# Kernel optimization log

Hardware: AMD Instinct MI355X
Metric: run time of the kernel (lower is better)

## Reference

```python
import jax, jax.numpy as jnp
import numpy as np

H, D = 8, 16
NA, NB, E, F = 50000, 50000, 200000, 128
SQRT_D = float(np.sqrt(D))


def _proj(x, W, b):
    # Linear then split heads: [N, F] -> [N, H, D]
    return (x @ W + b).reshape(x.shape[0], H, D)


def _seg_softmax(alpha, idx, n):
    # softmax over edges sharing the same destination node (per head)
    amax = jax.ops.segment_max(alpha, idx, num_segments=n)
    amax = jnp.where(jnp.isfinite(amax), amax, 0.0)
    ex = jnp.exp(alpha - amax[idx])
    den = jax.ops.segment_sum(ex, idx, num_segments=n)
    return ex / (den[idx] + 1e-16)


def _hgt_conv(xa, xb, eis, Wk, bk, Wq, bq, Wv, bv, Wa, ba, skip, arel, mrel, prel):
    # node types: 0='a', 1='b'; edge types: 0 a->b, 1 b->a, 2 a->a
    xs = (xa, xb)
    k = [_proj(xs[t], Wk[t], bk[t]) for t in range(2)]
    q = [_proj(xs[t], Wq[t], bq[t]) for t in range(2)]
    v = [_proj(xs[t], Wv[t], bv[t]) for t in range(2)]
    nn_ = (xa.shape[0], xb.shape[0])
    agg = [jnp.zeros((nn_[t], H, D), xa.dtype) for t in range(2)]
    spec = ((0, 1, eis[0]), (1, 0, eis[1]), (0, 0, eis[2]))
    for e, (s, d, ei) in enumerate(spec):
        src, dst = ei[0], ei[1]
        k_rel = jnp.einsum('nhd,hde->nhe', k[s], arel[e])  # [Ns,H,D]
        v_rel = jnp.einsum('nhd,hde->nhe', v[s], mrel[e])
        alpha = jnp.sum(q[d][dst] * k_rel[src], axis=-1) * prel[e] / SQRT_D  # [E,H]
        w = _seg_softmax(alpha, dst, nn_[d])
        agg[d] = agg[d] + jax.ops.segment_sum(v_rel[src] * w[..., None], dst, num_segments=nn_[d])
    outs = []
    for t in range(2):
        o = jax.nn.gelu(agg[t].reshape(-1, H * D), approximate=False) @ Wa[t] + ba[t]
        sgate = jax.nn.sigmoid(skip[t])  # learned skip-gate, dims match so always applied
        outs.append(sgate * o + (1.0 - sgate) * xs[t])
    return outs[0], outs[1]


def _forward(xa, xb, eis, Wk, bk, Wq, bq, Wv, bv, Wa, ba, skip, arel, mrel, prel):
    for l in range(2):
        xa, xb = _hgt_conv(xa, xb, eis, Wk[l], bk[l], Wq[l], bq[l], Wv[l], bv[l],
                           Wa[l], ba[l], skip[l], arel[l], mrel[l], prel[l])
        if l < 1:
            xa, xb = jax.nn.relu(xa), jax.nn.relu(xb)  # dropout: identity in eval mode
    return xa, xb


def setup_inputs() -> dict:
    key = jax.random.key(0)
    ks = jax.random.split(key, 12)
    s = 0.05
    return {
        'xa': jax.random.normal(ks[0], (NA, F), jnp.float32),
        'xb': jax.random.normal(ks[1], (NB, F), jnp.float32),
        'ei_ab': jax.random.randint(ks[2], (2, E), 0, NA, dtype=jnp.int32),
        'ei_ba': jax.random.randint(ks[3], (2, E), 0, NB, dtype=jnp.int32),
        'ei_aa': jax.random.randint(ks[4], (2, E), 0, NA, dtype=jnp.int32),
        'Wk': jax.random.normal(ks[5], (2, 2, F, F), jnp.float32) * s,
        'bk': jnp.zeros((2, 2, F), jnp.float32),
        'Wq': jax.random.normal(ks[6], (2, 2, F, F), jnp.float32) * s,
        'bq': jnp.zeros((2, 2, F), jnp.float32),
        'Wv': jax.random.normal(ks[7], (2, 2, F, F), jnp.float32) * s,
        'bv': jnp.zeros((2, 2, F), jnp.float32),
        'Wa': jax.random.normal(ks[8], (2, 2, F, F), jnp.float32) * s,
        'ba': jnp.zeros((2, 2, F), jnp.float32),
        'skip': jnp.zeros((2, 2), jnp.float32),
        'arel': jax.random.normal(ks[9], (2, 3, H, D, D), jnp.float32) * (1.0 / SQRT_D),
        'mrel': jax.random.normal(ks[10], (2, 3, H, D, D), jnp.float32) * (1.0 / SQRT_D),
        'prel': jnp.ones((2, 3, H), jnp.float32),
    }


def reference(xa, xb, ei_ab, ei_ba, ei_aa, Wk, bk, Wq, bq, Wv, bv, Wa, ba, skip, arel, mrel, prel):
    return _forward(xa, xb, (ei_ab, ei_ba, ei_aa), Wk, bk, Wq, bq, Wv, bv, Wa, ba, skip, arel, mrel, prel)
```

## Files before the change

kernel.cpp:

```cpp
#include <hip/hip_runtime.h>
#include <hip/hip_bf16.h>
#include <math.h>

#define F 128
#define NH 8
#define HD 16

static inline int cdiv(int a, int b) { return (a + b - 1) / b; }

typedef __attribute__((ext_vector_type(8))) short bf16x8;
typedef __attribute__((ext_vector_type(4))) float f32x4;

__device__ __forceinline__ float geluf(float x) {
    return 0.5f * x * (1.f + erff(x * 0.70710678118654752440f));
}

__device__ __forceinline__ short f2bf(float f) {
    __hip_bfloat16 h = __float2bfloat16(f);
    return *reinterpret_cast<short*>(&h);
}

__device__ __forceinline__ float bflo(unsigned int u) { return __uint_as_float(u << 16); }
__device__ __forceinline__ float bfhi(unsigned int u) { return __uint_as_float(u & 0xffff0000u); }
__device__ __forceinline__ float bf2f(short s) {
    return __uint_as_float(((unsigned int)(unsigned short)s) << 16);
}

__device__ __forceinline__ void slot_info(int slot, int& kind, int& wsel, int& e, int& t) {
    switch (slot) {
        case 0: kind = 0; wsel = 0; t = 0; e = 0; break;
        case 1: kind = 1; wsel = 1; t = 0; e = 0; break;
        case 2: kind = 1; wsel = 2; t = 0; e = 0; break;
        case 3: kind = 1; wsel = 1; t = 0; e = 2; break;
        case 4: kind = 1; wsel = 2; t = 0; e = 2; break;
        case 5: kind = 0; wsel = 0; t = 1; e = 0; break;
        case 6: kind = 1; wsel = 1; t = 1; e = 1; break;
        case 7: kind = 1; wsel = 2; t = 1; e = 1; break;
        case 8: kind = 0; wsel = 3; t = 0; e = 0; break;
        default: kind = 0; wsel = 3; t = 1; e = 0; break;
    }
}

__global__ void prep_weights(const float* __restrict__ Wk, const float* __restrict__ bk,
                             const float* __restrict__ Wq, const float* __restrict__ bq,
                             const float* __restrict__ Wv, const float* __restrict__ bv,
                             const float* __restrict__ Wa, const float* __restrict__ ba,
                             const float* __restrict__ arel, const float* __restrict__ mrel,
                             short* __restrict__ Wslots, float* __restrict__ bslots) {
    const int WTOT = 10 * 16384;
    const int layer = blockIdx.y;
    short* Wl = Wslots + (size_t)layer * WTOT;
    float* bl = bslots + (size_t)layer * 10 * 128;
    int idx = blockIdx.x * blockDim.x + threadIdx.x;
    if (idx < WTOT) {
        int slot = idx >> 14, rem = idx & 16383;
        int n = rem >> 7, k = rem & 127;
        int kind, wsel, e, t;
        slot_info(slot, kind, wsel, e, t);
        float out;
        if (kind == 0) {
            const float* Wb = (wsel == 0 ? Wq : Wa) + (size_t)(layer * 2 + t) * 16384;
            out = Wb[k * 128 + n];
        } else {
            int h = n >> 4, j = n & 15;
            const float* Wb = (wsel == 1 ? Wk : Wv) + (size_t)(layer * 2 + t) * 16384;
            const float* R = (wsel == 1 ? arel : mrel) + (size_t)((layer * 3 + e) * NH + h) * 256;
            float s = 0.f;
            #pragma unroll
            for (int d = 0; d < HD; ++d) s += Wb[k * 128 + h * 16 + d] * R[d * 16 + j];
            out = s;
        }
        Wl[(size_t)slot * 16384 + n * 128 + k] = f2bf(out);
    } else {
        int r = idx - WTOT;
        if (r < 10 * 128) {
            int slot = r >> 7, n = r & 127;
            int kind, wsel, e, t;
            slot_info(slot, kind, wsel, e, t);
            float out;
            if (kind == 0) {
                const float* bb = (wsel == 0 ? bq : ba) + (size_t)(layer * 2 + t) * 128;
                out = bb[n];
            } else {
                int h = n >> 4, j = n & 15;
                const float* bb = (wsel == 1 ? bk : bv) + (size_t)(layer * 2 + t) * 128;
                const float* R = (wsel == 1 ? arel : mrel) + (size_t)((layer * 3 + e) * NH + h) * 256;
                float s = 0.f;
                #pragma unroll
                for (int d = 0; d < HD; ++d) s += bb[h * 16 + d] * R[d * 16 + j];
                out = s;
            }
            bl[slot * 128 + n] = out;
        }
    }
}

template <typename AT>
__global__ __launch_bounds__(256) void gemm_qkv_all(
    const AT* __restrict__ Aa, const AT* __restrict__ Ab,
    const short* __restrict__ Wl, const float* __restrict__ bl,
    short* __restrict__ qA, short* __restrict__ kvA0, short* __restrict__ kvA2,
    short* __restrict__ qB, short* __restrict__ kvB1,
    int NA_, int NB_, int nbA) {
    __shared__ short Ws[128 * 136];
    __shared__ short As[64 * 136];
    float* Wsf = (float*)Ws;
    const int tid = threadIdx.x;
    const int bid = blockIdx.x;
    const int side = bid >= nbA;
    const AT* A = side ? Ab : Aa;
    const int N = side ? NB_ : NA_;
    const int row0 = (side ? bid - nbA : bid) * 64;
    const short* Wbase = Wl + (side ? (size_t)5 * 16384 : 0);
    const float* bbase = bl + (side ? 5 * 128 : 0);
    const int S = side ? 3 : 5;

    #pragma unroll
    for (int it = 0; it < 4; ++it) {
        int chunk = tid + it * 256;
        int r = chunk >> 4, c8 = (chunk & 15) * 8;
        int gr = row0 + r;
        bf16x8 s = {};
        if (gr < N) {
            if constexpr (sizeof(AT) == 4) {
                float4 v0 = *(const float4*)&A[(size_t)gr * F + c8];
                float4 v1 = *(const float4*)&A[(size_t)gr * F + c8 + 4];
                s[0] = f2bf(v0.x); s[1] = f2bf(v0.y); s[2] = f2bf(v0.z); s[3] = f2bf(v0.w);
                s[4] = f2bf(v1.x); s[5] = f2bf(v1.y); s[6] = f2bf(v1.z); s[7] = f2bf(v1.w);
            } else {
                s = *(const bf16x8*)&A[(size_t)gr * F + c8];
            }
        }
        *(bf16x8*)&As[r * 136 + c8] = s;
    }
    __syncthreads();

    const int wave = tid >> 6;
    const int lane = tid & 63;
    const int m16 = lane & 15;
    const int kg = lane >> 4;
    const int arow = wave * 16 + m16;

    bf16x8 af[4];
    #pragma unroll
    for (int kq = 0; kq < 4; ++kq)
        af[kq] = *(const bf16x8*)&As[arow * 136 + kq * 32 + kg * 8];

    for (int s = 0; s < S; ++s) {
        if (s) __syncthreads();
        const short* Wt = Wbase + (size_t)s * 16384;
        #pragma unroll
        for (int it = 0; it < 8; ++it) {
            int chunk = tid + it * 256;
            int r = chunk >> 4, c8 = (chunk & 15) * 8;
            *(int4*)&Ws[r * 136 + c8] = *(const int4*)&Wt[r * 128 + c8];
        }
        __syncthreads();

        f32x4 acc[8] = {};
        #pragma unroll
        for (int kq = 0; kq < 4; ++kq) {
            #pragma unroll
            for (int nt = 0; nt < 8; ++nt) {
                bf16x8 b = *(const bf16x8*)&Ws[(nt * 16 + m16) * 136 + kq * 32 + kg * 8];
                acc[nt] = __builtin_amdgcn_mfma_f32_16x16x32_bf16(af[kq], b, acc[nt], 0, 0, 0);
            }
        }
        __syncthreads();

        #pragma unroll
        for (int nt = 0; nt < 8; ++nt)
            #pragma unroll
            for (int r = 0; r < 4; ++r)
                Wsf[(wave * 16 + kg * 4 + r) * 132 + nt * 16 + m16] = acc[nt][r];
        __syncthreads();

        short* optr; int old, ooff;
        if (side) {
            if (s == 0)      { optr = qB;   old = 128; ooff = 0; }
            else if (s == 1) { optr = kvB1; old = 256; ooff = 0; }
            else             { optr = kvB1; old = 256; ooff = 128; }
        } else {
            if (s == 0)      { optr = qA;   old = 128; ooff = 0; }
            else if (s == 1) { optr = kvA0; old = 256; ooff = 0; }
            else if (s == 2) { optr = kvA0; old = 256; ooff = 128; }
            else if (s == 3) { optr = kvA2; old = 256; ooff = 0; }
            else             { optr = kvA2; old = 256; ooff = 128; }
        }
        const float* bias = bbase + s * 128;
        #pragma unroll
        for (int it = 0; it < 4; ++it) {
            int chunk = tid + it * 256;
            int r = chunk >> 4, c8 = (chunk & 15) * 8;
            int gr = row0 + r;
            if (gr >= N) continue;
            float4 b0 = *(const float4*)&bias[c8];
            float4 b1 = *(const float4*)&bias[c8 + 4];
            bf16x8 o;
            o[0] = f2bf(Wsf[r * 132 + c8 + 0] + b0.x);
            o[1] = f2bf(Wsf[r * 132 + c8 + 1] + b0.y);
            o[2] = f2bf(Wsf[r * 132 + c8 + 2] + b0.z);
            o[3] = f2bf(Wsf[r * 132 + c8 + 3] + b0.w);
            o[4] = f2bf(Wsf[r * 132 + c8 + 4] + b1.x);
            o[5] = f2bf(Wsf[r * 132 + c8 + 5] + b1.y);
            o[6] = f2bf(Wsf[r * 132 + c8 + 6] + b1.z);
            o[7] = f2bf(Wsf[r * 132 + c8 + 7] + b1.w);
            *(bf16x8*)&optr[(size_t)gr * old + ooff + c8] = o;
        }
    }
}

template <int OMODE>
__global__ __launch_bounds__(256) void gemm_out_all(
    const short* __restrict__ aggA, const short* __restrict__ aggB,
    const short* __restrict__ Wl, const float* __restrict__ bl,
    const float* __restrict__ xfA, const float* __restrict__ xfB,
    const short* __restrict__ xbA, const short* __restrict__ xbB,
    const float* __restrict__ skipp,
    float* __restrict__ CfA, float* __restrict__ CfB,
    short* __restrict__ CbA, short* __restrict__ CbB,
    int NA_, int NB_, int nbA) {
    __shared__ short Ws[128 * 136];
    __shared__ short As[64 * 136];
    float* Wsf = (float*)Ws;
    const int tid = threadIdx.x;
    const int bid = blockIdx.x;
    const int side = bid >= nbA;
    const short* A = side ? aggB : aggA;
    const int N = side ? NB_ : NA_;
    const int row0 = (side ? bid - nbA : bid) * 64;
    const short* Wt = Wl + (size_t)(side ? 9 : 8) * 16384;
    const float* bias = bl + (side ? 9 : 8) * 128;

    #pragma unroll
    for (int it = 0; it < 8; ++it) {
        int chunk = tid + it * 256;
        int r = chunk >> 4, c8 = (chunk & 15) * 8;
        *(int4*)&Ws[r * 136 + c8] = *(const int4*)&Wt[r * 128 + c8];
    }
    #pragma unroll
    for (int it = 0; it < 4; ++it) {
        int chunk = tid + it * 256;
        int r = chunk >> 4, c8 = (chunk & 15) * 8;
        int gr = row0 + r;
        bf16x8 s = {};
        if (gr < N) {
            s = *(const bf16x8*)&A[(size_t)gr * F + c8];
            #pragma unroll
            for (int u = 0; u < 8; ++u) s[u] = f2bf(geluf(bf2f(s[u])));
        }
        *(bf16x8*)&As[r * 136 + c8] = s;
    }
    __syncthreads();

    const int wave = tid >> 6;
    const int lane = tid & 63;
    const int m16 = lane & 15;
    const int kg = lane >> 4;
    const int arow = wave * 16 + m16;

    f32x4 acc[8] = {};
    #pragma unroll
    for (int k0 = 0; k0 < 128; k0 += 32) {
        bf16x8 a = *(const bf16x8*)&As[arow * 136 + k0 + kg * 8];
        #pragma unroll
        for (int nt = 0; nt < 8; ++nt) {
            bf16x8 b = *(const bf16x8*)&Ws[(nt * 16 + m16) * 136 + k0 + kg * 8];
            acc[nt] = __builtin_amdgcn_mfma_f32_16x16x32_bf16(a, b, acc[nt], 0, 0, 0);
        }
    }
    __syncthreads();

    #pragma unroll
    for (int nt = 0; nt < 8; ++nt)
        #pragma unroll
        for (int r = 0; r < 4; ++r)
            Wsf[(wave * 16 + kg * 4 + r) * 132 + nt * 16 + m16] = acc[nt][r];
    __syncthreads();

    float sg = 1.f / (1.f + expf(-skipp[side]));
    #pragma unroll
    for (int it = 0; it < 4; ++it) {
        int chunk = tid + it * 256;
        int r = chunk >> 4, c8 = (chunk & 15) * 8;
        int gr = row0 + r;
        if (gr >= N) continue;
        float4 b0 = *(const float4*)&bias[c8];
        float4 b1 = *(const float4*)&bias[c8 + 4];
        float v[8];
        #pragma unroll
        for (int u = 0; u < 8; ++u) v[u] = Wsf[r * 132 + c8 + u];
        v[0] += b0.x; v[1] += b0.y; v[2] += b0.z; v[3] += b0.w;
        v[4] += b1.x; v[5] += b1.y; v[6] += b1.z; v[7] += b1.w;
        if (OMODE == 1) {
            const float* xf = side ? xfB : xfA;
            float4 x0 = *(const float4*)&xf[(size_t)gr * F + c8];
            float4 x1 = *(const float4*)&xf[(size_t)gr * F + c8 + 4];
            float xr[8] = {x0.x, x0.y, x0.z, x0.w, x1.x, x1.y, x1.z, x1.w};
            bf16x8 o;
            #pragma unroll
            for (int u = 0; u < 8; ++u)
                o[u] = f2bf(fmaxf(sg * v[u] + (1.f - sg) * xr[u], 0.f));
            *(bf16x8*)&(side ? CbB : CbA)[(size_t)gr * F + c8] = o;
        } else {
            const short* xb = side ? xbB : xbA;
            bf16x8 xrv = *(const bf16x8*)&xb[(size_t)gr * F + c8];
            float* Cf = side ? CfB : CfA;
            float o[8];
            #pragma unroll
            for (int u = 0; u < 8; ++u)
                o[u] = sg * v[u] + (1.f - sg) * bf2f(xrv[u]);
            *(float4*)&Cf[(size_t)gr * F + c8]     = make_float4(o[0], o[1], o[2], o[3]);
            *(float4*)&Cf[(size_t)gr * F + c8 + 4] = make_float4(o[4], o[5], o[6], o[7]);
        }
    }
}


__global__ void hist_all(const int* __restrict__ ei0, const int* __restrict__ ei1,
                         const int* __restrict__ ei2, int E0, int E1, int E2,
                         int NB_, int NA_, int* __restrict__ cnt) {
    int i = blockIdx.x * 256 + threadIdx.x;
    if (i >= E0 + E1 + E2) return;
    const int* ei; int li, Ee, base;
    if (i < E0)           { li = i;           ei = ei0; Ee = E0; base = 0; }
    else if (i < E0 + E1) { li = i - E0;      ei = ei1; Ee = E1; base = NB_; }
    else                  { li = i - E0 - E1; ei = ei2; Ee = E2; base = NB_ + NA_; }
    atomicAdd(&cnt[base + ei[Ee + li]], 1);
}

__global__ void scan1(const int* __restrict__ cnt, int n, int* __restrict__ off,
                      int* __restrict__ bsum) {
    __shared__ int lds[256];
    int tid = threadIdx.x, i = blockIdx.x * 256 + tid;
    int v = (i < n) ? cnt[i] : 0;
    lds[tid] = v;
    __syncthreads();
    #pragma unroll
    for (int s = 1; s < 256; s <<= 1) {
        int t = (tid >= s) ? lds[tid - s] : 0;
        __syncthreads();
        lds[tid] += t;
        __syncthreads();
    }
    if (i < n) off[i] = lds[tid] - v;
    if (tid == 255) bsum[blockIdx.x] = lds[255];
}

__global__ __launch_bounds__(1024) void scan2(int* __restrict__ bsum, int nb,
                                              int* __restrict__ off_n) {
    __shared__ int lds[1024];
    int tid = threadIdx.x;
    int v = (tid < nb) ? bsum[tid] : 0;
    lds[tid] = v;
    __syncthreads();
    #pragma unroll
    for (int s = 1; s < 1024; s <<= 1) {
        int t = (tid >= s) ? lds[tid - s] : 0;
        __syncthreads();
        lds[tid] += t;
        __syncthreads();
    }
    if (tid < nb) bsum[tid] = lds[tid] - v;
    if (tid == 1023) *off_n = lds[1023];
}

__global__ void scan3(int* __restrict__ off, int* __restrict__ woff,
                      const int* __restrict__ bsum, int n) {
    int i = blockIdx.x * 256 + threadIdx.x;
    if (i < n) {
        int v = off[i] + bsum[blockIdx.x];
        off[i] = v;
        woff[i] = v;
    }
}

__global__ void scatter_all(const int* __restrict__ ei0, const int* __restrict__ ei1,
                            const int* __restrict__ ei2, int E0, int E1, int E2,
                            int NB_, int NA_, int* __restrict__ woff,
                            int* __restrict__ csr_src) {
    int i = blockIdx.x * 256 + threadIdx.x;
    if (i >= E0 + E1 + E2) return;
    const int* ei; int li, Ee, base;
    if (i < E0)           { li = i;           ei = ei0; Ee = E0; base = 0; }
    else if (i < E0 + E1) { li = i - E0;      ei = ei1; Ee = E1; base = NB_; }
    else                  { li = i - E0 - E1; ei = ei2; Ee = E2; base = NB_ + NA_; }
    int p = atomicAdd(&woff[base + ei[Ee + li]], 1);
    csr_src[p] = ei[li] * 128;
}

#define CH 8
template <int NSET>
__device__ __forceinline__ void seg_attn_core(
    const unsigned int* __restrict__ q32,
    const unsigned int* __restrict__ kv1, const int* __restrict__ off1,
    const unsigned int* __restrict__ kv2, const int* __restrict__ off2,
    const int* __restrict__ csr_src,
    const float* __restrict__ prel1, const float* __restrict__ prel2,
    unsigned int* __restrict__ agg32, int Nd, int blk) {
    int dst = blk * 4 + (threadIdx.x >> 6);
    if (dst >= Nd) return;
    int l = threadIdx.x & 63;
    int h = l >> 3;
    unsigned int qu = q32[(size_t)dst * 64 + l];
    float qlo = bflo(qu), qhi = bfhi(qu);
    float rlo = 0.f, rhi = 0.f;
    #pragma unroll
    for (int s = 0; s < NSET; ++s) {
        const unsigned int* kv = s ? kv2 : kv1;
        const int* off = s ? off2 : off1;
        float pr = (s ? prel2[h] : prel1[h]) * 0.25f;
        int e0 = off[dst], e1 = off[dst + 1];
        float m = -INFINITY, den = 0.f, alo = 0.f, ahi = 0.f;
        for (int base = e0; base < e1; base += CH) {
            int n = e1 - base; if (n > CH) n = CH;
            float al[CH];
            unsigned int vu[CH];
            float cmax = -INFINITY;
            if (n == CH) {
                int sj[CH];
                unsigned int ku[CH];
                #pragma unroll
                for (int c = 0; c < CH; ++c) sj[c] = csr_src[base + c];
                #pragma unroll
                for (int c = 0; c < CH; ++c) {
                    ku[c] = kv[sj[c] + l];
                    vu[c] = kv[sj[c] + 64 + l];
                }
                #pragma unroll
                for (int c = 0; c < CH; ++c) {
                    float p = bflo(ku[c]) * qlo + bfhi(ku[c]) * qhi;
                    p += __shfl_xor(p, 4, 8);
                    p += __shfl_xor(p, 2, 8);
                    p += __shfl_xor(p, 1, 8);
                    al[c] = p * pr;
                    cmax = fmaxf(cmax, al[c]);
                }
            } else {
                int sj[CH];
                unsigned int ku[CH];
                #pragma unroll
                for (int c = 0; c < CH; ++c) if (c < n) sj[c] = csr_src[base + c];
                #pragma unroll
                for (int c = 0; c < CH; ++c) if (c < n) {
                    ku[c] = kv[sj[c] + l];
                    vu[c] = kv[sj[c] + 64 + l];
                }
                #pragma unroll
                for (int c = 0; c < CH; ++c) if (c < n) {
                    float p = bflo(ku[c]) * qlo + bfhi(ku[c]) * qhi;
                    p += __shfl_xor(p, 4, 8);
                    p += __shfl_xor(p, 2, 8);
                    p += __shfl_xor(p, 1, 8);
                    al[c] = p * pr;
                    cmax = fmaxf(cmax, al[c]);
                }
            }
            float nm = fmaxf(m, cmax);
            float corr = __expf(m - nm);
            den *= corr; alo *= corr; ahi *= corr;
            if (n == CH) {
                #pragma unroll
                for (int c = 0; c < CH; ++c) {
                    float ex = __expf(al[c] - nm);
                    den += ex;
                    alo = fmaf(ex, bflo(vu[c]), alo);
                    ahi = fmaf(ex, bfhi(vu[c]), ahi);
                }
            } else {
                #pragma unroll
                for (int c = 0; c < CH; ++c) if (c < n) {
                    float ex = __expf(al[c] - nm);
                    den += ex;
                    alo = fmaf(ex, bflo(vu[c]), alo);
                    ahi = fmaf(ex, bfhi(vu[c]), ahi);
                }
            }
            m = nm;
        }
        float inv = 1.f / (den + 1e-16f);
        rlo = fmaf(alo, inv, rlo);
        rhi = fmaf(ahi, inv, rhi);
    }
    unsigned int plo = (unsigned int)(unsigned short)f2bf(rlo);
    unsigned int phi = (unsigned int)(unsigned short)f2bf(rhi);
    agg32[(size_t)dst * 64 + l] = plo | (phi << 16);
}

__global__ __launch_bounds__(256) void seg_attn_all(
    const short* __restrict__ qA, const short* __restrict__ kvA0,
    const short* __restrict__ kvA2, const short* __restrict__ qB,
    const short* __restrict__ kvB1,
    const int* __restrict__ off0, const int* __restrict__ off1,
    const int* __restrict__ off2, const int* __restrict__ csrS,
    const float* __restrict__ prelL,
    short* __restrict__ aggA, short* __restrict__ aggB,
    int NA_, int NB_, int nba) {
    if ((int)blockIdx.x < nba) {
        seg_attn_core<2>((const unsigned int*)qA,
                         (const unsigned int*)kvB1, off1,
                         (const unsigned int*)kvA2, off2, csrS,
                         prelL + 1 * NH, prelL + 2 * NH,
                         (unsigned int*)aggA, NA_, blockIdx.x);
    } else {
        seg_attn_core<1>((const unsigned int*)qB,
                         (const unsigned int*)kvA0, off0,
                         nullptr, nullptr, csrS,
                         prelL + 0 * NH, nullptr,
                         (unsigned int*)aggB, NB_, blockIdx.x - nba);
    }
}

extern "C" void kernel_launch(void* const* d_in, const int* in_sizes, int n_in,
                              void* d_out, int out_size, void* d_ws, size_t ws_size,
                              hipStream_t stream) {
    const float* xa   = (const float*)d_in[0];
    const float* xb   = (const float*)d_in[1];
    const int* ei_ab  = (const int*)d_in[2];
    const int* ei_ba  = (const int*)d_in[3];
    const int* ei_aa  = (const int*)d_in[4];
    const float* Wk   = (const float*)d_in[5];
    const float* bk   = (const float*)d_in[6];
    const float* Wq   = (const float*)d_in[7];
    const float* bq   = (const float*)d_in[8];
    const float* Wv   = (const float*)d_in[9];
    const float* bv   = (const float*)d_in[10];
    const float* Wa   = (const float*)d_in[11];
    const float* ba   = (const float*)d_in[12];
    const float* skip = (const float*)d_in[13];
    const float* arel = (const float*)d_in[14];
    const float* mrel = (const float*)d_in[15];
    const float* prel = (const float*)d_in[16];

    const int NA = in_sizes[0] / F;
    const int NB = in_sizes[1] / F;
    const int E0 = in_sizes[2] / 2, E1 = in_sizes[3] / 2, E2 = in_sizes[4] / 2;
    const int ET = E0 + E1 + E2;
    const int NT = NB + NA + NA;

    float* ws = (float*)d_ws;
    size_t o = 0;
    float* bslots = ws + o; o += 2 * 10 * 128;
    int* iws = (int*)(ws + o);
    size_t io = 0;
    int* cnt   = iws + io; io += NT;
    int* bsum  = iws + io; io += 1024;
    int* offc  = iws + io; io += NT + 1;
    int* woff  = iws + io; io += NT;
    int* csrS  = iws + io; io += ET;
    io = (io + 7) & ~(size_t)7;
    short* sws = (short*)(iws + io);
    size_t so = 0;
    short* qA   = sws + so; so += (size_t)NA * 128;
    short* kvA0 = sws + so; so += (size_t)NA * 256;
    short* kvA2 = sws + so; so += (size_t)NA * 256;
    short* qB   = sws + so; so += (size_t)NB * 128;
    short* kvB1 = sws + so; so += (size_t)NB * 256;
    short* aggA = sws + so; so += (size_t)NA * 128;
    short* aggB = sws + so; so += (size_t)NB * 128;
    short* x1ab = sws + so; so += (size_t)NA * 128;
    short* x1bb = sws + so; so += (size_t)NB * 128;
    short* Wslots = sws + so; so += (size_t)2 * 10 * 16384;

    float* outA = (float*)d_out;
    float* outB = (float*)d_out + (size_t)NA * F;

    {
        dim3 g(cdiv(10 * 16384 + 10 * 128, 256), 2);
        prep_weights<<<g, 256, 0, stream>>>(Wk, bk, Wq, bq, Wv, bv, Wa, ba,
                                            arel, mrel, Wslots, bslots);
    }

    hipMemsetAsync(cnt, 0, (size_t)NT * sizeof(int), stream);
    hist_all<<<cdiv(ET, 256), 256, 0, stream>>>(ei_ab, ei_ba, ei_aa, E0, E1, E2, NB, NA, cnt);
    {
        int nb = cdiv(NT, 256);
        scan1<<<nb, 256, 0, stream>>>(cnt, NT, offc, bsum);
        scan2<<<1, 1024, 0, stream>>>(bsum, nb, offc + NT);
        scan3<<<nb, 256, 0, stream>>>(offc, woff, bsum, NT);
    }
    scatter_all<<<cdiv(ET, 256), 256, 0, stream>>>(ei_ab, ei_ba, ei_aa, E0, E1, E2, NB, NA, woff, csrS);

    const int* off_e0 = offc;
    const int* off_e1 = offc + NB;
    const int* off_e2 = offc + NB + NA;

    const int nbA64 = cdiv(NA, 64), nbB64 = cdiv(NB, 64);
    const int nba4 = cdiv(NA, 4), nbb4 = cdiv(NB, 4);

    for (int l = 0; l < 2; ++l) {
        const short* Wl = Wslots + (size_t)l * 10 * 16384;
        const float* bl = bslots + (size_t)l * 10 * 128;

        if (l == 0) {
            gemm_qkv_all<float><<<nbA64 + nbB64, 256, 0, stream>>>(
                xa, xb, Wl, bl, qA, kvA0, kvA2, qB, kvB1, NA, NB, nbA64);
        } else {
            gemm_qkv_all<short><<<nbA64 + nbB64, 256, 0, stream>>>(
                x1ab, x1bb, Wl, bl, qA, kvA0, kvA2, qB, kvB1, NA, NB, nbA64);
        }

        seg_attn_all<<<nba4 + nbb4, 256, 0, stream>>>(
            qA, kvA0, kvA2, qB, kvB1, off_e0, off_e1, off_e2, csrS,
            prel + (size_t)l * 3 * NH, aggA, aggB, NA, NB, nba4);

        if (l == 0) {
            gemm_out_all<1><<<nbA64 + nbB64, 256, 0, stream>>>(
                aggA, aggB, Wl, bl, xa, xb, nullptr, nullptr,
                skip + 0, nullptr, nullptr, x1ab, x1bb, NA, NB, nbA64);
        } else {
            gemm_out_all<0><<<nbA64 + nbB64, 256, 0, stream>>>(
                aggA, aggB, Wl, bl, nullptr, nullptr, x1ab, x1bb,
                skip + 2, outA, outB, nullptr, nullptr, NA, NB, nbA64);
        }
    }
}
```

Before: 381.9 us.

## Fuse layer-0 output GEMM with layer-1 QKV GEMM and interleave dual-relation attention

Merges the layer-0 output projection (GELU, skip gate, ReLU) with the layer-1 QKV projection in one kernel. The freshly computed x1 tile stays in shared memory as the A operand, so one launch and a global re-read of x1 are avoided. It also rewrites the two-relation segment attention to walk both edge sets in the same loop, so their gathers are issued together for more memory-level parallelism. The cost is higher register pressure in the attention kernel and a longer fused GEMM kernel that reloads weights for five slots.

```diff
diff --git a/kernel.cpp b/kernel.cpp
--- a/kernel.cpp
+++ b/kernel.cpp
@@ -95,9 +95,24 @@
     }
 }
 
-template <typename AT>
+__device__ __forceinline__ void qkv_slot_ptr(int side, int s,
+    short* qA, short* kvA0, short* kvA2, short* qB, short* kvB1,
+    short*& optr, int& old, int& ooff) {
+    if (side) {
+        if (s == 0)      { optr = qB;   old = 128; ooff = 0; }
+        else if (s == 1) { optr = kvB1; old = 256; ooff = 0; }
+        else             { optr = kvB1; old = 256; ooff = 128; }
+    } else {
+        if (s == 0)      { optr = qA;   old = 128; ooff = 0; }
+        else if (s == 1) { optr = kvA0; old = 256; ooff = 0; }
+        else if (s == 2) { optr = kvA0; old = 256; ooff = 128; }
+        else if (s == 3) { optr = kvA2; old = 256; ooff = 0; }
+        else             { optr = kvA2; old = 256; ooff = 128; }
+    }
+}
+
 __global__ __launch_bounds__(256) void gemm_qkv_all(
-    const AT* __restrict__ Aa, const AT* __restrict__ Ab,
+    const float* __restrict__ Aa, const float* __restrict__ Ab,
     const short* __restrict__ Wl, const float* __restrict__ bl,
     short* __restrict__ qA, short* __restrict__ kvA0, short* __restrict__ kvA2,
     short* __restrict__ qB, short* __restrict__ kvB1,
@@ -108,7 +123,7 @@
     const int tid = threadIdx.x;
     const int bid = blockIdx.x;
     const int side = bid >= nbA;
-    const AT* A = side ? Ab : Aa;
+    const float* A = side ? Ab : Aa;
     const int N = side ? NB_ : NA_;
     const int row0 = (side ? bid - nbA : bid) * 64;
     const short* Wbase = Wl + (side ? (size_t)5 * 16384 : 0);
@@ -122,14 +137,10 @@
         int gr = row0 + r;
         bf16x8 s = {};
         if (gr < N) {
-            if constexpr (sizeof(AT) == 4) {
-                float4 v0 = *(const float4*)&A[(size_t)gr * F + c8];
-                float4 v1 = *(const float4*)&A[(size_t)gr * F + c8 + 4];
-                s[0] = f2bf(v0.x); s[1] = f2bf(v0.y); s[2] = f2bf(v0.z); s[3] = f2bf(v0.w);
-                s[4] = f2bf(v1.x); s[5] = f2bf(v1.y); s[6] = f2bf(v1.z); s[7] = f2bf(v1.w);
-            } else {
-                s = *(const bf16x8*)&A[(size_t)gr * F + c8];
-            }
+            float4 v0 = *(const float4*)&A[(size_t)gr * F + c8];
+            float4 v1 = *(const float4*)&A[(size_t)gr * F + c8 + 4];
+            s[0] = f2bf(v0.x); s[1] = f2bf(v0.y); s[2] = f2bf(v0.z); s[3] = f2bf(v0.w);
+            s[4] = f2bf(v1.x); s[5] = f2bf(v1.y); s[6] = f2bf(v1.z); s[7] = f2bf(v1.w);
         }
         *(bf16x8*)&As[r * 136 + c8] = s;
     }
@@ -176,17 +187,7 @@
         __syncthreads();
 
         short* optr; int old, ooff;
-        if (side) {
-            if (s == 0)      { optr = qB;   old = 128; ooff = 0; }
-            else if (s == 1) { optr = kvB1; old = 256; ooff = 0; }
-            else             { optr = kvB1; old = 256; ooff = 128; }
-        } else {
-            if (s == 0)      { optr = qA;   old = 128; ooff = 0; }
-            else if (s == 1) { optr = kvA0; old = 256; ooff = 0; }
-            else if (s == 2) { optr = kvA0; old = 256; ooff = 128; }
-            else if (s == 3) { optr = kvA2; old = 256; ooff = 0; }
-            else             { optr = kvA2; old = 256; ooff = 128; }
-        }
+        qkv_slot_ptr(side, s, qA, kvA0, kvA2, qB, kvB1, optr, old, ooff);
         const float* bias = bbase + s * 128;
         #pragma unroll
         for (int it = 0; it < 4; ++it) {
@@ -210,15 +211,174 @@
     }
 }
 
-template <int OMODE>
-__global__ __launch_bounds__(256) void gemm_out_all(
+__global__ __launch_bounds__(256) void fused_out_qkv(
+    const short* __restrict__ aggA, const short* __restrict__ aggB,
+    const short* __restrict__ Wl0, const float* __restrict__ bl0,
+    const float* __restrict__ xfA, const float* __restrict__ xfB,
+    const float* __restrict__ skipp,
+    const short* __restrict__ Wl1, const float* __restrict__ bl1,
+    short* __restrict__ x1A, short* __restrict__ x1B,
+    short* __restrict__ qA, short* __restrict__ kvA0, short* __restrict__ kvA2,
+    short* __restrict__ qB, short* __restrict__ kvB1,
+    int NA_, int NB_, int nbA) {
+    __shared__ short Ws[128 * 136];
+    __shared__ short As[64 * 136];
+    float* Wsf = (float*)Ws;
+    const int tid = threadIdx.x;
+    const int bid = blockIdx.x;
+    const int side = bid >= nbA;
+    const short* A = side ? aggB : aggA;
+    const int N = side ? NB_ : NA_;
+    const int row0 = (side ? bid - nbA : bid) * 64;
+    const short* Wt0 = Wl0 + (size_t)(side ? 9 : 8) * 16384;
+    const float* bias0 = bl0 + (side ? 9 : 8) * 128;
+
+    #pragma unroll
+    for (int it = 0; it < 8; ++it) {
+        int chunk = tid + it * 256;
+        int r = chunk >> 4, c8 = (chunk & 15) * 8;
+        *(int4*)&Ws[r * 136 + c8] = *(const int4*)&Wt0[r * 128 + c8];
+    }
+    #pragma unroll
+    for (int it = 0; it < 4; ++it) {
+        int chunk = tid + it * 256;
+        int r = chunk >> 4, c8 = (chunk & 15) * 8;
+        int gr = row0 + r;
+        bf16x8 s = {};
+        if (gr < N) {
+            s = *(const bf16x8*)&A[(size_t)gr * F + c8];
+            #pragma unroll
+            for (int u = 0; u < 8; ++u) s[u] = f2bf(geluf(bf2f(s[u])));
+        }
+        *(bf16x8*)&As[r * 136 + c8] = s;
+    }
+    __syncthreads();
+
+    const int wave = tid >> 6;
+    const int lane = tid & 63;
+    const int m16 = lane & 15;
+    const int kg = lane >> 4;
+    const int arow = wave * 16 + m16;
+
+    {
+        f32x4 acc[8] = {};
+        #pragma unroll
+        for (int k0 = 0; k0 < 128; k0 += 32) {
+            bf16x8 a = *(const bf16x8*)&As[arow * 136 + k0 + kg * 8];
+            #pragma unroll
+            for (int nt = 0; nt < 8; ++nt) {
+                bf16x8 b = *(const bf16x8*)&Ws[(nt * 16 + m16) * 136 + k0 + kg * 8];
+                acc[nt] = __builtin_amdgcn_mfma_f32_16x16x32_bf16(a, b, acc[nt], 0, 0, 0);
+            }
+        }
+        __syncthreads();
+        #pragma unroll
+        for (int nt = 0; nt < 8; ++nt)
+            #pragma unroll
+            for (int r = 0; r < 4; ++r)
+                Wsf[(wave * 16 + kg * 4 + r) * 132 + nt * 16 + m16] = acc[nt][r];
+        __syncthreads();
+    }
+
+    {
+        float sg = 1.f / (1.f + expf(-skipp[side]));
+        short* x1 = side ? x1B : x1A;
+        const float* xf = side ? xfB : xfA;
+        #pragma unroll
+        for (int it = 0; it < 4; ++it) {
+            int chunk = tid + it * 256;
+            int r = chunk >> 4, c8 = (chunk & 15) * 8;
+            int gr = row0 + r;
+            if (gr >= N) continue;
+            float4 b0 = *(const float4*)&bias0[c8];
+            float4 b1 = *(const float4*)&bias0[c8 + 4];
+            float4 x0v = *(const float4*)&xf[(size_t)gr * F + c8];
+            float4 x1v = *(const float4*)&xf[(size_t)gr * F + c8 + 4];
+            float v[8];
+            #pragma unroll
+            for (int u = 0; u < 8; ++u) v[u] = Wsf[r * 132 + c8 + u];
+            v[0] += b0.x; v[1] += b0.y; v[2] += b0.z; v[3] += b0.w;
+            v[4] += b1.x; v[5] += b1.y; v[6] += b1.z; v[7] += b1.w;
+            float xr[8] = {x0v.x, x0v.y, x0v.z, x0v.w, x1v.x, x1v.y, x1v.z, x1v.w};
+            bf16x8 o;
+            #pragma unroll
+            for (int u = 0; u < 8; ++u)
+                o[u] = f2bf(fmaxf(sg * v[u] + (1.f - sg) * xr[u], 0.f));
+            *(bf16x8*)&x1[(size_t)gr * F + c8] = o;
+            *(bf16x8*)&As[r * 136 + c8] = o;
+        }
+    }
+    __syncthreads();
+
+    bf16x8 af[4];
+    #pragma unroll
+    for (int kq = 0; kq < 4; ++kq)
+        af[kq] = *(const bf16x8*)&As[arow * 136 + kq * 32 + kg * 8];
+
+    const short* Wbase = Wl1 + (side ? (size_t)5 * 16384 : 0);
+    const float* bbase = bl1 + (side ? 5 * 128 : 0);
+    const int S = side ? 3 : 5;
+
+    for (int s = 0; s < S; ++s) {
+        __syncthreads();
+        const short* Wt = Wbase + (size_t)s * 16384;
+        #pragma unroll
+        for (int it = 0; it < 8; ++it) {
+            int chunk = tid + it * 256;
+            int r = chunk >> 4, c8 = (chunk & 15) * 8;
+            *(int4*)&Ws[r * 136 + c8] = *(const int4*)&Wt[r * 128 + c8];
+        }
+        __syncthreads();
+
+        f32x4 acc[8] = {};
+        #pragma unroll
+        for (int kq = 0; kq < 4; ++kq) {
+            #pragma unroll
+            for (int nt = 0; nt < 8; ++nt) {
+                bf16x8 b = *(const bf16x8*)&Ws[(nt * 16 + m16) * 136 + kq * 32 + kg * 8];
+                acc[nt] = __builtin_amdgcn_mfma_f32_16x16x32_bf16(af[kq], b, acc[nt], 0, 0, 0);
+            }
+        }
+        __syncthreads();
+
+        #pragma unroll
+        for (int nt = 0; nt < 8; ++nt)
+            #pragma unroll
+            for (int r = 0; r < 4; ++r)
+                Wsf[(wave * 16 + kg * 4 + r) * 132 + nt * 16 + m16] = acc[nt][r];
+        __syncthreads();
+
+        short* optr; int old, ooff;
+        qkv_slot_ptr(side, s, qA, kvA0, kvA2, qB, kvB1, optr, old, ooff);
+        const float* bias = bbase + s * 128;
+        #pragma unroll
+        for (int it = 0; it < 4; ++it) {
+            int chunk = tid + it * 256;
+            int r = chunk >> 4, c8 = (chunk & 15) * 8;
+            int gr = row0 + r;
+            if (gr >= N) continue;
+            float4 b0 = *(const float4*)&bias[c8];
+            float4 b1 = *(const float4*)&bias[c8 + 4];
+            bf16x8 o;
+            o[0] = f2bf(Wsf[r * 132 + c8 + 0] + b0.x);
+            o[1] = f2bf(Wsf[r * 132 + c8 + 1] + b0.y);
+            o[2] = f2bf(Wsf[r * 132 + c8 + 2] + b0.z);
+            o[3] = f2bf(Wsf[r * 132 + c8 + 3] + b0.w);
+            o[4] = f2bf(Wsf[r * 132 + c8 + 4] + b1.x);
+            o[5] = f2bf(Wsf[r * 132 + c8 + 5] + b1.y);
+            o[6] = f2bf(Wsf[r * 132 + c8 + 6] + b1.z);
+            o[7] = f2bf(Wsf[r * 132 + c8 + 7] + b1.w);
+            *(bf16x8*)&optr[(size_t)gr * old + ooff + c8] = o;
+        }
+    }
+}
+
+__global__ __launch_bounds__(256) void gemm_out_final(
     const short* __restrict__ aggA, const short* __restrict__ aggB,
     const short* __restrict__ Wl, const float* __restrict__ bl,
-    const float* __restrict__ xfA, const float* __restrict__ xfB,
     const short* __restrict__ xbA, const short* __restrict__ xbB,
     const float* __restrict__ skipp,
     float* __restrict__ CfA, float* __restrict__ CfB,
-    short* __restrict__ CbA, short* __restrict__ CbB,
     int NA_, int NB_, int nbA) {
     __shared__ short Ws[128 * 136];
     __shared__ short As[64 * 136];
@@ -292,27 +452,15 @@
         for (int u = 0; u < 8; ++u) v[u] = Wsf[r * 132 + c8 + u];
         v[0] += b0.x; v[1] += b0.y; v[2] += b0.z; v[3] += b0.w;
         v[4] += b1.x; v[5] += b1.y; v[6] += b1.z; v[7] += b1.w;
-        if (OMODE == 1) {
-            const float* xf = side ? xfB : xfA;
-            float4 x0 = *(const float4*)&xf[(size_t)gr * F + c8];
-            float4 x1 = *(const float4*)&xf[(size_t)gr * F + c8 + 4];
-            float xr[8] = {x0.x, x0.y, x0.z, x0.w, x1.x, x1.y, x1.z, x1.w};
-            bf16x8 o;
-            #pragma unroll
-            for (int u = 0; u < 8; ++u)
-                o[u] = f2bf(fmaxf(sg * v[u] + (1.f - sg) * xr[u], 0.f));
-            *(bf16x8*)&(side ? CbB : CbA)[(size_t)gr * F + c8] = o;
-        } else {
-            const short* xb = side ? xbB : xbA;
-            bf16x8 xrv = *(const bf16x8*)&xb[(size_t)gr * F + c8];
-            float* Cf = side ? CfB : CfA;
-            float o[8];
-            #pragma unroll
-            for (int u = 0; u < 8; ++u)
-                o[u] = sg * v[u] + (1.f - sg) * bf2f(xrv[u]);
-            *(float4*)&Cf[(size_t)gr * F + c8]     = make_float4(o[0], o[1], o[2], o[3]);
-            *(float4*)&Cf[(size_t)gr * F + c8 + 4] = make_float4(o[4], o[5], o[6], o[7]);
-        }
+        const short* xb = side ? xbB : xbA;
+        bf16x8 xrv = *(const bf16x8*)&xb[(size_t)gr * F + c8];
+        float* Cf = side ? CfB : CfA;
+        float o[8];
+        #pragma unroll
+        for (int u = 0; u < 8; ++u)
+            o[u] = sg * v[u] + (1.f - sg) * bf2f(xrv[u]);
+        *(float4*)&Cf[(size_t)gr * F + c8]     = make_float4(o[0], o[1], o[2], o[3]);
+        *(float4*)&Cf[(size_t)gr * F + c8 + 4] = make_float4(o[4], o[5], o[6], o[7]);
     }
 }
 
@@ -390,8 +538,63 @@
 }
 
 #define CH 8
-template <int NSET>
-__device__ __forceinline__ void seg_attn_core(
+
+__device__ __forceinline__ void seg_attn_one(
+    const unsigned int* __restrict__ q32,
+    const unsigned int* __restrict__ kv1, const int* __restrict__ off1,
+    const int* __restrict__ csr_src, const float* __restrict__ prel1,
+    unsigned int* __restrict__ agg32, int Nd, int blk) {
+    int dst = blk * 4 + (threadIdx.x >> 6);
+    if (dst >= Nd) return;
+    int l = threadIdx.x & 63;
+    int h = l >> 3;
+    unsigned int qu = q32[(size_t)dst * 64 + l];
+    float qlo = bflo(qu), qhi = bfhi(qu);
+    float pr = prel1[h] * 0.25f;
+    int c0 = off1[dst], e0 = off1[dst + 1];
+    float m = -INFINITY, den = 0.f, alo = 0.f, ahi = 0.f;
+    while (c0 < e0) {
+        int n = e0 - c0; if (n > CH) n = CH;
+        int sj[CH];
+        unsigned int ku[CH], vu[CH];
+        #pragma unroll
+        for (int c = 0; c < CH; ++c) if (c < n) sj[c] = csr_src[c0 + c];
+        #pragma unroll
+        for (int c = 0; c < CH; ++c) if (c < n) {
+            ku[c] = kv1[sj[c] + l];
+            vu[c] = kv1[sj[c] + 64 + l];
+        }
+        float al[CH];
+        float cmax = -INFINITY;
+        #pragma unroll
+        for (int c = 0; c < CH; ++c) if (c < n) {
+            float p = bflo(ku[c]) * qlo + bfhi(ku[c]) * qhi;
+            p += __shfl_xor(p, 4, 8);
+            p += __shfl_xor(p, 2, 8);
+            p += __shfl_xor(p, 1, 8);
+            al[c] = p * pr;
+            cmax = fmaxf(cmax, al[c]);
+        }
+        float nm = fmaxf(m, cmax);
+        float corr = __expf(m - nm);
+        den *= corr; alo *= corr; ahi *= corr;
+        #pragma unroll
+        for (int c = 0; c < CH; ++c) if (c < n) {
+            float ex = __expf(al[c] - nm);
+            den += ex;
+            alo = fmaf(ex, bflo(vu[c]), alo);
+            ahi = fmaf(ex, bfhi(vu[c]), ahi);
+        }
+        m = nm;
+        c0 += n;
+    }
+    float inv = 1.f / (den + 1e-16f);
+    unsigned int plo = (unsigned int)(unsigned short)f2bf(alo * inv);
+    unsigned int phi = (unsigned int)(unsigned short)f2bf(ahi * inv);
+    agg32[(size_t)dst * 64 + l] = plo | (phi << 16);
+}
+
+__device__ __forceinline__ void seg_attn_dual(
     const unsigned int* __restrict__ q32,
     const unsigned int* __restrict__ kv1, const int* __restrict__ off1,
     const unsigned int* __restrict__ kv2, const int* __restrict__ off2,
@@ -404,84 +607,90 @@
     int h = l >> 3;
     unsigned int qu = q32[(size_t)dst * 64 + l];
     float qlo = bflo(qu), qhi = bfhi(qu);
-    float rlo = 0.f, rhi = 0.f;
-    #pragma unroll
-    for (int s = 0; s < NSET; ++s) {
-        const unsigned int* kv = s ? kv2 : kv1;
-        const int* off = s ? off2 : off1;
-        float pr = (s ? prel2[h] : prel1[h]) * 0.25f;
-        int e0 = off[dst], e1 = off[dst + 1];
-        float m = -INFINITY, den = 0.f, alo = 0.f, ahi = 0.f;
-        for (int base = e0; base < e1; base += CH) {
-            int n = e1 - base; if (n > CH) n = CH;
+    float pr0 = prel1[h] * 0.25f;
+    float pr1 = prel2[h] * 0.25f;
+    int c0 = off1[dst], e0 = off1[dst + 1];
+    int c1 = off2[dst], e1 = off2[dst + 1];
+    float m0 = -INFINITY, d0 = 0.f, lo0 = 0.f, hi0 = 0.f;
+    float m1 = -INFINITY, d1 = 0.f, lo1 = 0.f, hi1 = 0.f;
+    while (c0 < e0 || c1 < e1) {
+        int n0 = e0 - c0; if (n0 > CH) n0 = CH; if (n0 < 0) n0 = 0;
+        int n1 = e1 - c1; if (n1 > CH) n1 = CH; if (n1 < 0) n1 = 0;
+        unsigned int ku0[CH], vu0[CH], ku1[CH], vu1[CH];
+        {
+            int sj[CH];
+            #pragma unroll
+            for (int c = 0; c < CH; ++c) if (c < n0) sj[c] = csr_src[c0 + c];
+            #pragma unroll
+            for (int c = 0; c < CH; ++c) if (c < n0) {
+                ku0[c] = kv1[sj[c] + l];
+                vu0[c] = kv1[sj[c] + 64 + l];
+            }
+        }
+        {
+            int sj[CH];
+            #pragma unroll
+            for (int c = 0; c < CH; ++c) if (c < n1) sj[c] = csr_src[c1 + c];
+            #pragma unroll
+            for (int c = 0; c < CH; ++c) if (c < n1) {
+                ku1[c] = kv2[sj[c] + l];
+                vu1[c] = kv2[sj[c] + 64 + l];
+            }
+        }
+        if (n0 > 0) {
             float al[CH];
-            unsigned int vu[CH];
             float cmax = -INFINITY;
-            if (n == CH) {
-                int sj[CH];
-                unsigned int ku[CH];
-                #pragma unroll
-                for (int c = 0; c < CH; ++c) sj[c] = csr_src[base + c];
-                #pragma unroll
-                for (int c = 0; c < CH; ++c) {
-                    ku[c] = kv[sj[c] + l];
-                    vu[c] = kv[sj[c] + 64 + l];
-                }
-                #pragma unroll
-                for (int c = 0; c < CH; ++c) {
-                    float p = bflo(ku[c]) * qlo + bfhi(ku[c]) * qhi;
-                    p += __shfl_xor(p, 4, 8);
-                    p += __shfl_xor(p, 2, 8);
-                    p += __shfl_xor(p, 1, 8);
-                    al[c] = p * pr;
-                    cmax = fmaxf(cmax, al[c]);
-                }
-            } else {
-                int sj[CH];
-                unsigned int ku[CH];
-                #pragma unroll
-                for (int c = 0; c < CH; ++c) if (c < n) sj[c] = csr_src[base + c];
-                #pragma unroll
-                for (int c = 0; c < CH; ++c) if (c < n) {
-                    ku[c] = kv[sj[c] + l];
-                    vu[c] = kv[sj[c] + 64 + l];
-                }
-                #pragma unroll
-                for (int c = 0; c < CH; ++c) if (c < n) {
-                    float p = bflo(ku[c]) * qlo + bfhi(ku[c]) * qhi;
-                    p += __shfl_xor(p, 4, 8);
-                    p += __shfl_xor(p, 2, 8);
-                    p += __shfl_xor(p, 1, 8);
-                    al[c] = p * pr;
-                    cmax = fmaxf(cmax, al[c]);
-                }
-            }
-            float nm = fmaxf(m, cmax);
-            float corr = __expf(m - nm);
-            den *= corr; alo *= corr; ahi *= corr;
-            if (n == CH) {
-                #pragma unroll
-                for (int c = 0; c < CH; ++c) {
-                    float ex = __expf(al[c] - nm);
-                    den += ex;
-                    alo = fmaf(ex, bflo(vu[c]), alo);
-                    ahi = fmaf(ex, bfhi(vu[c]), ahi);
-                }
-            } else {
-                #pragma unroll
-                for (int c = 0; c < CH; ++c) if (c < n) {
-                    float ex = __expf(al[c] - nm);
-                    den += ex;
-                    alo = fmaf(ex, bflo(vu[c]), alo);
-                    ahi = fmaf(ex, bfhi(vu[c]), ahi);
-                }
-            }
-            m = nm;
-        }
-        float inv = 1.f / (den + 1e-16f);
-        rlo = fmaf(alo, inv, rlo);
-        rhi = fmaf(ahi, inv, rhi);
-    }
+            #pragma unroll
+            for (int c = 0; c < CH; ++c) if (c < n0) {
+                float p = bflo(ku0[c]) * qlo + bfhi(ku0[c]) * qhi;
+                p += __shfl_xor(p, 4, 8);
+                p += __shfl_xor(p, 2, 8);
+                p += __shfl_xor(p, 1, 8);
+                al[c] = p * pr0;
+                cmax = fmaxf(cmax, al[c]);
+            }
+            float nm = fmaxf(m0, cmax);
+            float corr = __expf(m0 - nm);
+            d0 *= corr; lo0 *= corr; hi0 *= corr;
+            #pragma unroll
+            for (int c = 0; c < CH; ++c) if (c < n0) {
+                float ex = __expf(al[c] - nm);
+                d0 += ex;
+                lo0 = fmaf(ex, bflo(vu0[c]), lo0);
+                hi0 = fmaf(ex, bfhi(vu0[c]), hi0);
+            }
+            m0 = nm;
+        }
+        if (n1 > 0) {
+            float al[CH];
+            float cmax = -INFINITY;
+            #pragma unroll
+            for (int c = 0; c < CH; ++c) if (c < n1) {
+                float p = bflo(ku1[c]) * qlo + bfhi(ku1[c]) * qhi;
+                p += __shfl_xor(p, 4, 8);
+                p += __shfl_xor(p, 2, 8);
+                p += __shfl_xor(p, 1, 8);
+                al[c] = p * pr1;
+                cmax = fmaxf(cmax, al[c]);
+            }
+            float nm = fmaxf(m1, cmax);
+            float corr = __expf(m1 - nm);
+            d1 *= corr; lo1 *= corr; hi1 *= corr;
+            #pragma unroll
+            for (int c = 0; c < CH; ++c) if (c < n1) {
+                float ex = __expf(al[c] - nm);
+                d1 += ex;
+                lo1 = fmaf(ex, bflo(vu1[c]), lo1);
+                hi1 = fmaf(ex, bfhi(vu1[c]), hi1);
+            }
+            m1 = nm;
+        }
+        c0 += n0; c1 += n1;
+    }
+    float inv0 = 1.f / (d0 + 1e-16f);
+    float inv1 = 1.f / (d1 + 1e-16f);
+    float rlo = lo0 * inv0 + lo1 * inv1;
+    float rhi = hi0 * inv0 + hi1 * inv1;
     unsigned int plo = (unsigned int)(unsigned short)f2bf(rlo);
     unsigned int phi = (unsigned int)(unsigned short)f2bf(rhi);
     agg32[(size_t)dst * 64 + l] = plo | (phi << 16);
@@ -497,17 +706,16 @@
     short* __restrict__ aggA, short* __restrict__ aggB,
     int NA_, int NB_, int nba) {
     if ((int)blockIdx.x < nba) {
-        seg_attn_core<2>((const unsigned int*)qA,
-                         (const unsigned int*)kvB1, off1,
-                         (const unsigned int*)kvA2, off2, csrS,
-                         prelL + 1 * NH, prelL + 2 * NH,
-                         (unsigned int*)aggA, NA_, blockIdx.x);
+        seg_attn_dual((const unsigned int*)qA,
+                      (const unsigned int*)kvB1, off1,
+                      (const unsigned int*)kvA2, off2, csrS,
+                      prelL + 1 * NH, prelL + 2 * NH,
+                      (unsigned int*)aggA, NA_, blockIdx.x);
     } else {
-        seg_attn_core<1>((const unsigned int*)qB,
-                         (const unsigned int*)kvA0, off0,
-                         nullptr, nullptr, csrS,
-                         prelL + 0 * NH, nullptr,
-                         (unsigned int*)aggB, NB_, blockIdx.x - nba);
+        seg_attn_one((const unsigned int*)qB,
+                     (const unsigned int*)kvA0, off0, csrS,
+                     prelL + 0 * NH,
+                     (unsigned int*)aggB, NB_, blockIdx.x - nba);
     }
 }
 
@@ -588,30 +796,26 @@
     const int nbA64 = cdiv(NA, 64), nbB64 = cdiv(NB, 64);
     const int nba4 = cdiv(NA, 4), nbb4 = cdiv(NB, 4);
 
-    for (int l = 0; l < 2; ++l) {
-        const short* Wl = Wslots + (size_t)l * 10 * 16384;
-        const float* bl = bslots + (size_t)l * 10 * 128;
-
-        if (l == 0) {
-            gemm_qkv_all<float><<<nbA64 + nbB64, 256, 0, stream>>>(
-                xa, xb, Wl, bl, qA, kvA0, kvA2, qB, kvB1, NA, NB, nbA64);
-        } else {
-            gemm_qkv_all<short><<<nbA64 + nbB64, 256, 0, stream>>>(
-                x1ab, x1bb, Wl, bl, qA, kvA0, kvA2, qB, kvB1, NA, NB, nbA64);
-        }
-
-        seg_attn_all<<<nba4 + nbb4, 256, 0, stream>>>(
-            qA, kvA0, kvA2, qB, kvB1, off_e0, off_e1, off_e2, csrS,
-            prel + (size_t)l * 3 * NH, aggA, aggB, NA, NB, nba4);
-
-        if (l == 0) {
-            gemm_out_all<1><<<nbA64 + nbB64, 256, 0, stream>>>(
-                aggA, aggB, Wl, bl, xa, xb, nullptr, nullptr,
-                skip + 0, nullptr, nullptr, x1ab, x1bb, NA, NB, nbA64);
-        } else {
-            gemm_out_all<0><<<nbA64 + nbB64, 256, 0, stream>>>(
-                aggA, aggB, Wl, bl, nullptr, nullptr, x1ab, x1bb,
-                skip + 2, outA, outB, nullptr, nullptr, NA, NB, nbA64);
-        }
-    }
-}
+    const short* Wl0 = Wslots;
+    const short* Wl1 = Wslots + (size_t)10 * 16384;
+    const float* bl0 = bslots;
+    const float* bl1 = bslots + 10 * 128;
+
+    gemm_qkv_all<<<nbA64 + nbB64, 256, 0, stream>>>(
+        xa, xb, Wl0, bl0, qA, kvA0, kvA2, qB, kvB1, NA, NB, nbA64);
+
+    seg_attn_all<<<nba4 + nbb4, 256, 0, stream>>>(
+        qA, kvA0, kvA2, qB, kvB1, off_e0, off_e1, off_e2, csrS,
+        prel, aggA, aggB, NA, NB, nba4);
+
+    fused_out_qkv<<<nbA64 + nbB64, 256, 0, stream>>>(
+        aggA, aggB, Wl0, bl0, xa, xb, skip, Wl1, bl1,
+        x1ab, x1bb, qA, kvA0, kvA2, qB, kvB1, NA, NB, nbA64);
+
+    seg_attn_all<<<nba4 + nbb4, 256, 0, stream>>>(
+        qA, kvA0, kvA2, qB, kvB1, off_e0, off_e1, off_e2, csrS,
+        prel + 3 * NH, aggA, aggB, NA, NB, nba4);
+
+    gemm_out_final<<<nbA64 + nbB64, 256, 0, stream>>>(
+        aggA, aggB, Wl1, bl1, x1ab, x1bb, skip + 2, outA, outB, NA, NB, nbA64);
+}
```

New measurement: 421.3 us. +10.3%, slower.
